# Optimization experiments

Hardware: AMD Instinct MI355X
Metric: run time of the kernel (lower is better)

## Reference

```python
import jax, jax.numpy as jnp
import numpy as np

PROX_TOL = 5
SEG_PENALTY = 3.0
SEG_REWARD = 0.3
CLASS_WEIGHTS = np.array([0.1, 5.0, 5.0], dtype=np.float32)


def setup_inputs() -> dict:
    key = jax.random.key(0)
    k1, k2, k3 = jax.random.split(key, 3)
    B, S, C = 256, 16384, 3
    logits = jax.random.normal(k1, (B, S, C), dtype=jnp.float32)
    labels = jax.random.randint(k2, (B, S), 0, 3, dtype=jnp.int64)
    tokens = jax.random.randint(k3, (B, S), 0, 1000, dtype=jnp.int64)
    return {"logits": logits, "labels": labels, "tokens": tokens}


def _window_any(mask, tol):
    # sliding 'any' over [t-tol, t+tol], clipped at sequence edges ('SAME' padding)
    m = mask.astype(jnp.float32)
    r = jax.lax.reduce_window(m, 0.0, jax.lax.max, (1, 2 * tol + 1), (1, 1), 'SAME')
    return r > 0.0


def reference(logits, labels, tokens):
    B, S, C = logits.shape
    cw = jnp.asarray(CLASS_WEIGHTS, dtype=logits.dtype)

    # weighted cross-entropy, reduction='none' -> w[y] * nll  [B, S]
    logp = jax.nn.log_softmax(logits, axis=-1)
    nll = -jnp.take_along_axis(logp, labels[..., None], axis=-1)[..., 0]
    base_loss = nll * cw[labels]

    predictions = jnp.argmax(logits, axis=-1)
    pred_switch = predictions >= 1   # [B, S]
    true_switch = labels >= 1        # [B, S]

    # segmentation adjustment (tokens is not None): for predicted switches,
    # the t+1 < S check overwrites the penalty with the reward, so:
    #   t <  S-1        -> reward
    #   t == S-1, t>=1  -> penalty (offset loop fired)
    pos = jnp.arange(S)
    adj = jnp.where(pred_switch & (pos < S - 1), SEG_REWARD,
                    jnp.where(pred_switch & (pos == S - 1) & (pos >= 1), SEG_PENALTY, 1.0))
    base_loss = base_loss * adj.astype(base_loss.dtype)

    # proximity reward: true switch with any predicted switch within +/- tol -> *0.1
    pred_near = _window_any(pred_switch, PROX_TOL)
    base_loss = jnp.where(true_switch & pred_near, base_loss * 0.1, base_loss)

    # false-positive penalty: predicted switch farther than tol from every true
    # switch -> *2.0 (only applied if the sequence has at least one true switch)
    true_near = _window_any(true_switch, PROX_TOL)
    has_true = jnp.any(true_switch, axis=1, keepdims=True)
    base_loss = jnp.where(pred_switch & has_true & (~true_near), base_loss * 2.0, base_loss)

    valid_mask = (labels != -100).astype(base_loss.dtype)
    return (base_loss * valid_mask).sum() / valid_mask.sum()
```

## Files before the change

### kernel.cpp

```cpp
#include <hip/hip_runtime.h>

#define SEQ 16384
#define TOL 5
#define CHUNK 1024
#define NCHUNK (SEQ / CHUNK)
#define NW (CHUNK / 64)
#define JITER (CHUNK / 256)
#define NROW 256
#define NBLK (NROW * NCHUNK)
#define TOTAL_VALID 4194304.0


__global__ __launch_bounds__(256, 4) void switch_loss_kernel(
    const float* __restrict__ logits,
    const int* __restrict__ labels,
    float* __restrict__ blk_sum, float* __restrict__ blk_fp,
    int* __restrict__ blk_any)
{
    const int row = blockIdx.y;
    const int chunk = blockIdx.x;
    const int s0 = chunk * CHUNK;
    const int t = threadIdx.x;
    const int w = t >> 6;
    const int lane = t & 63;

    __shared__ unsigned long long ps[NW + 2];
    __shared__ unsigned long long ts[NW + 2];
    __shared__ float wsum[4], wfp[4];
    __shared__ int wany[4];

    const float* __restrict__ lrow = logits + (size_t)row * (SEQ * 3);
    const int* __restrict__ labrow = labels + (size_t)row * SEQ;

    float l0v[JITER], l1v[JITER], l2v[JITER];
    int yv[JITER];
    #pragma unroll
    for (int j = 0; j < JITER; ++j) {
        const int s = s0 + j * 256 + t;
        l0v[j] = lrow[s * 3 + 0];
        l1v[j] = lrow[s * 3 + 1];
        l2v[j] = lrow[s * 3 + 2];
        yv[j]  = labrow[s];
    }

    if (w == 0) {
        const int pos = s0 - 64 + lane;
        const bool act = (lane >= 64 - TOL) && (pos >= 0);
        bool psw = false, tsw = false;
        if (act) {
            const float h0 = lrow[pos * 3 + 0];
            const float h1 = lrow[pos * 3 + 1];
            const float h2 = lrow[pos * 3 + 2];
            psw = (h1 > h0) || (h2 > fmaxf(h0, h1));
            const int y = labrow[pos];
            tsw = (y >= 1) && (y <= 2);
        }
        const unsigned long long bp = __ballot(psw);
        const unsigned long long bt = __ballot(tsw);
        if (lane == 0) { ps[0] = bp; ts[0] = bt; }
    } else if (w == 1) {
        const int pos = s0 + CHUNK + lane;
        const bool act = (lane < TOL) && (pos < SEQ);
        bool psw = false, tsw = false;
        if (act) {
            const float h0 = lrow[pos * 3 + 0];
            const float h1 = lrow[pos * 3 + 1];
            const float h2 = lrow[pos * 3 + 2];
            psw = (h1 > h0) || (h2 > fmaxf(h0, h1));
            const int y = labrow[pos];
            tsw = (y >= 1) && (y <= 2);
        }
        const unsigned long long bp = __ballot(psw);
        const unsigned long long bt = __ballot(tsw);
        if (lane == 0) { ps[NW + 1] = bp; ts[NW + 1] = bt; }
    }

    float lossv[JITER];
    unsigned pswbits = 0, tswbits = 0;
    unsigned long long my_ts_or = 0ull;

    #pragma unroll
    for (int j = 0; j < JITER; ++j) {
        const int s = s0 + j * 256 + t;
        const float l0 = l0v[j], l1 = l1v[j], l2 = l2v[j];
        const int y = yv[j];

        const float m01 = fmaxf(l0, l1);
        const float m = fmaxf(m01, l2);
        const bool psw = (l1 > l0) || (l2 > m01);

        const float sum = __expf(l0 - m) + __expf(l1 - m) + __expf(l2 - m);
        const float lse = m + __logf(sum);

        const bool valid = (y >= 0) && (y <= 2);
        const bool tsw = valid && (y >= 1);
        const float ly = (y == 0) ? l0 : ((y == 1) ? l1 : l2);
        const float wgt = (y == 0) ? 0.1f : 5.0f;
        float loss = valid ? (lse - ly) * wgt : 0.0f;

        const float adj = psw ? ((s < SEQ - 1) ? 0.3f : 3.0f) : 1.0f;
        lossv[j] = loss * adj;

        pswbits |= (unsigned)psw << j;
        tswbits |= (unsigned)tsw << j;

        const unsigned long long bp = __ballot(psw);
        const unsigned long long bt = __ballot(tsw);
        my_ts_or |= bt;
        if (lane == 0) { ps[1 + j * 4 + w] = bp; ts[1 + j * 4 + w] = bt; }
    }
    if (lane == 0) wany[w] = (my_ts_or != 0ull) ? 1 : 0;
    __syncthreads();

    float lsum = 0.0f, lfp = 0.0f;

    #pragma unroll
    for (int j = 0; j < JITER; ++j) {
        const int s = s0 + j * 256 + t;
        const bool psw = (pswbits >> j) & 1u;
        const bool tsw = (tswbits >> j) & 1u;

        int lo = s - TOL; lo = (lo < 0) ? 0 : lo;
        int hi = s + TOL; hi = (hi > SEQ - 1) ? (SEQ - 1) : hi;
        const int len = hi - lo + 1;
        const int rel = lo - s0 + 64;
        const int qq = rel >> 6;
        const int sh = rel & 63;

        unsigned long long pw = ps[qq] >> sh;
        unsigned long long tw = ts[qq] >> sh;
        if (sh + len > 64) {
            pw |= ps[qq + 1] << (64 - sh);
            tw |= ts[qq + 1] << (64 - sh);
        }
        const unsigned long long mlen = (1ull << len) - 1ull;
        const bool pred_near = (pw & mlen) != 0ull;
        const bool true_near = (tw & mlen) != 0ull;

        float loss = lossv[j];
        if (tsw && pred_near) loss *= 0.1f;
        lsum += loss;
        if (psw && !true_near) lfp += loss;
    }

    #pragma unroll
    for (int off = 32; off > 0; off >>= 1) {
        lsum += __shfl_down(lsum, off, 64);
        lfp  += __shfl_down(lfp, off, 64);
    }
    if (lane == 0) { wsum[w] = lsum; wfp[w] = lfp; }
    __syncthreads();
    if (t == 0) {
        const int slot = row * NCHUNK + chunk;
        blk_sum[slot] = wsum[0] + wsum[1] + wsum[2] + wsum[3];
        blk_fp[slot]  = wfp[0] + wfp[1] + wfp[2] + wfp[3];
        blk_any[slot] = wany[0] | wany[1] | wany[2] | wany[3];
    }
}

__global__ void finalize_kernel(const float* __restrict__ blk_sum,
                                const float* __restrict__ blk_fp,
                                const int* __restrict__ blk_any,
                                float* __restrict__ out) {
    const int t = threadIdx.x;
    const int w = t >> 6, lane = t & 63;
    __shared__ double wsum[4];

    float s = 0.0f, f = 0.0f;
    int any = 0;
    #pragma unroll
    for (int c = 0; c < NCHUNK; ++c) {
        const int slot = t * NCHUNK + c;
        s += blk_sum[slot];
        f += blk_fp[slot];
        any |= blk_any[slot];
    }
    double v = (double)s + (any ? (double)f : 0.0);
    #pragma unroll
    for (int off = 32; off > 0; off >>= 1)
        v += __shfl_down(v, off, 64);
    if (lane == 0) wsum[w] = v;
    __syncthreads();
    if (t == 0)
        out[0] = (float)((wsum[0] + wsum[1] + wsum[2] + wsum[3]) / TOTAL_VALID);
}

extern "C" void kernel_launch(void* const* d_in, const int* in_sizes, int n_in,
                              void* d_out, int out_size, void* d_ws, size_t ws_size,
                              hipStream_t stream) {
    const float* logits = (const float*)d_in[0];
    const int* labels = (const int*)d_in[1];
    (void)in_sizes; (void)n_in; (void)out_size; (void)ws_size;

    float* blk_sum = (float*)d_ws;
    float* blk_fp = blk_sum + NBLK;
    int* blk_any = (int*)(blk_fp + NBLK);
    float* out = (float*)d_out;

    switch_loss_kernel<<<dim3(NCHUNK, NROW), 256, 0, stream>>>(
        logits, labels, blk_sum, blk_fp, blk_any);
    finalize_kernel<<<1, 256, 0, stream>>>(blk_sum, blk_fp, blk_any, out);
}
```

Before: 108.2 us.

## Vectorize loads with 8 contiguous positions per thread and byte-packed switch masks

Each thread now handles 8 consecutive positions and loads its logits as six float4 values and its labels as two int4 values, instead of strided scalar loads. The chunk doubles to 2048 positions, so there are half as many blocks. Switch bits are packed into per-thread bytes in shared memory and assembled into 64-bit words, which replaces the per-iteration wave ballots. Halo loading is merged into one wave, and finalize uses vector loads. The aim is fewer, wider memory transactions, at the cost of non-coalesced per-thread 96-byte strides and fewer blocks in flight.

```diff
diff --git a/kernel.cpp b/kernel.cpp
--- a/kernel.cpp
+++ b/kernel.cpp
@@ -2,10 +2,10 @@
 
 #define SEQ 16384
 #define TOL 5
-#define CHUNK 1024
+#define CHUNK 2048
 #define NCHUNK (SEQ / CHUNK)
 #define NW (CHUNK / 64)
-#define JITER (CHUNK / 256)
+#define P 8
 #define NROW 256
 #define NBLK (NROW * NCHUNK)
 #define TOTAL_VALID 4194304.0
@@ -26,71 +26,61 @@
 
     __shared__ unsigned long long ps[NW + 2];
     __shared__ unsigned long long ts[NW + 2];
+    __shared__ __align__(8) unsigned char psb[256];
+    __shared__ __align__(8) unsigned char tsb[256];
     __shared__ float wsum[4], wfp[4];
     __shared__ int wany[4];
 
     const float* __restrict__ lrow = logits + (size_t)row * (SEQ * 3);
     const int* __restrict__ labrow = labels + (size_t)row * SEQ;
 
-    float l0v[JITER], l1v[JITER], l2v[JITER];
-    int yv[JITER];
-    #pragma unroll
-    for (int j = 0; j < JITER; ++j) {
-        const int s = s0 + j * 256 + t;
-        l0v[j] = lrow[s * 3 + 0];
-        l1v[j] = lrow[s * 3 + 1];
-        l2v[j] = lrow[s * 3 + 2];
-        yv[j]  = labrow[s];
-    }
-
-    if (w == 0) {
-        const int pos = s0 - 64 + lane;
-        const bool act = (lane >= 64 - TOL) && (pos >= 0);
-        bool psw = false, tsw = false;
-        if (act) {
+    const int sb = s0 + t * P;
+
+    const float4* __restrict__ lp = (const float4*)(lrow + (size_t)sb * 3);
+    const float4 f0 = lp[0], f1 = lp[1], f2 = lp[2], f3 = lp[3], f4 = lp[4], f5 = lp[5];
+    const int4* __restrict__ yp = (const int4*)(labrow + sb);
+    const int4 ya = yp[0], yb = yp[1];
+
+    bool hp = false, ht = false;
+    if (t < 2 * TOL) {
+        const int pos = (t < TOL) ? (s0 - TOL + t) : (s0 + CHUNK + (t - TOL));
+        if (pos >= 0 && pos < SEQ) {
             const float h0 = lrow[pos * 3 + 0];
             const float h1 = lrow[pos * 3 + 1];
             const float h2 = lrow[pos * 3 + 2];
-            psw = (h1 > h0) || (h2 > fmaxf(h0, h1));
-            const int y = labrow[pos];
-            tsw = (y >= 1) && (y <= 2);
+            hp = (h1 > h0) || (h2 > fmaxf(h0, h1));
+            ht = (labrow[pos] >= 1);
         }
-        const unsigned long long bp = __ballot(psw);
-        const unsigned long long bt = __ballot(tsw);
-        if (lane == 0) { ps[0] = bp; ts[0] = bt; }
-    } else if (w == 1) {
-        const int pos = s0 + CHUNK + lane;
-        const bool act = (lane < TOL) && (pos < SEQ);
-        bool psw = false, tsw = false;
-        if (act) {
-            const float h0 = lrow[pos * 3 + 0];
-            const float h1 = lrow[pos * 3 + 1];
-            const float h2 = lrow[pos * 3 + 2];
-            psw = (h1 > h0) || (h2 > fmaxf(h0, h1));
-            const int y = labrow[pos];
-            tsw = (y >= 1) && (y <= 2);
+    }
+    if (w == 0) {
+        const unsigned long long bp = __ballot(hp);
+        const unsigned long long bt = __ballot(ht);
+        if (lane == 0) {
+            ps[0] = (bp & 0x1Full) << 59;
+            ts[0] = (bt & 0x1Full) << 59;
+            ps[NW + 1] = (bp >> TOL) & 0x1Full;
+            ts[NW + 1] = (bt >> TOL) & 0x1Full;
         }
-        const unsigned long long bp = __ballot(psw);
-        const unsigned long long bt = __ballot(tsw);
-        if (lane == 0) { ps[NW + 1] = bp; ts[NW + 1] = bt; }
-    }
-
-    float lossv[JITER];
-    unsigned pswbits = 0, tswbits = 0;
-    unsigned long long my_ts_or = 0ull;
-
-    #pragma unroll
-    for (int j = 0; j < JITER; ++j) {
-        const int s = s0 + j * 256 + t;
-        const float l0 = l0v[j], l1 = l1v[j], l2 = l2v[j];
-        const int y = yv[j];
+    }
+
+    const float L0[P] = {f0.x, f0.w, f1.z, f2.y, f3.x, f3.w, f4.z, f5.y};
+    const float L1[P] = {f0.y, f1.x, f1.w, f2.z, f3.y, f4.x, f4.w, f5.z};
+    const float L2[P] = {f0.z, f1.y, f2.x, f2.w, f3.z, f4.y, f5.x, f5.w};
+    const int   Y[P]  = {ya.x, ya.y, ya.z, ya.w, yb.x, yb.y, yb.z, yb.w};
+
+    float lossv[P];
+    unsigned pn = 0, tn = 0;
+    #pragma unroll
+    for (int p = 0; p < P; ++p) {
+        const float l0 = L0[p], l1 = L1[p], l2 = L2[p];
+        const int y = Y[p];
 
         const float m01 = fmaxf(l0, l1);
-        const float m = fmaxf(m01, l2);
+        const float mx = fmaxf(m01, l2);
         const bool psw = (l1 > l0) || (l2 > m01);
 
-        const float sum = __expf(l0 - m) + __expf(l1 - m) + __expf(l2 - m);
-        const float lse = m + __logf(sum);
+        const float sum = __expf(l0 - mx) + __expf(l1 - mx) + __expf(l2 - mx);
+        const float lse = mx + __logf(sum);
 
         const bool valid = (y >= 0) && (y <= 2);
         const bool tsw = valid && (y >= 1);
@@ -98,27 +88,33 @@
         const float wgt = (y == 0) ? 0.1f : 5.0f;
         float loss = valid ? (lse - ly) * wgt : 0.0f;
 
+        const int s = sb + p;
         const float adj = psw ? ((s < SEQ - 1) ? 0.3f : 3.0f) : 1.0f;
-        lossv[j] = loss * adj;
-
-        pswbits |= (unsigned)psw << j;
-        tswbits |= (unsigned)tsw << j;
-
-        const unsigned long long bp = __ballot(psw);
-        const unsigned long long bt = __ballot(tsw);
-        my_ts_or |= bt;
-        if (lane == 0) { ps[1 + j * 4 + w] = bp; ts[1 + j * 4 + w] = bt; }
-    }
-    if (lane == 0) wany[w] = (my_ts_or != 0ull) ? 1 : 0;
+        lossv[p] = loss * adj;
+
+        pn |= (unsigned)psw << p;
+        tn |= (unsigned)tsw << p;
+    }
+    psb[t] = (unsigned char)pn;
+    tsb[t] = (unsigned char)tn;
+    {
+        const unsigned long long ba = __ballot(tn != 0);
+        if (lane == 0) wany[w] = (ba != 0ull) ? 1 : 0;
+    }
+    __syncthreads();
+
+    if (t < NW) {
+        ps[1 + t] = *(const unsigned long long*)&psb[t * 8];
+        ts[1 + t] = *(const unsigned long long*)&tsb[t * 8];
+    }
     __syncthreads();
 
     float lsum = 0.0f, lfp = 0.0f;
-
-    #pragma unroll
-    for (int j = 0; j < JITER; ++j) {
-        const int s = s0 + j * 256 + t;
-        const bool psw = (pswbits >> j) & 1u;
-        const bool tsw = (tswbits >> j) & 1u;
+    #pragma unroll
+    for (int p = 0; p < P; ++p) {
+        const int s = sb + p;
+        const bool psw = (pn >> p) & 1u;
+        const bool tsw = (tn >> p) & 1u;
 
         int lo = s - TOL; lo = (lo < 0) ? 0 : lo;
         int hi = s + TOL; hi = (hi > SEQ - 1) ? (SEQ - 1) : hi;
@@ -137,7 +133,7 @@
         const bool pred_near = (pw & mlen) != 0ull;
         const bool true_near = (tw & mlen) != 0ull;
 
-        float loss = lossv[j];
+        float loss = lossv[p];
         if (tsw && pred_near) loss *= 0.1f;
         lsum += loss;
         if (psw && !true_near) lfp += loss;
@@ -164,25 +160,27 @@
                                 float* __restrict__ out) {
     const int t = threadIdx.x;
     const int w = t >> 6, lane = t & 63;
-    __shared__ double wsum[4];
-
-    float s = 0.0f, f = 0.0f;
-    int any = 0;
-    #pragma unroll
-    for (int c = 0; c < NCHUNK; ++c) {
-        const int slot = t * NCHUNK + c;
-        s += blk_sum[slot];
-        f += blk_fp[slot];
-        any |= blk_any[slot];
-    }
+    __shared__ double wsumd[4];
+
+    const float4* __restrict__ fs = (const float4*)(blk_sum + t * NCHUNK);
+    const float4* __restrict__ ff = (const float4*)(blk_fp + t * NCHUNK);
+    const int4* __restrict__ fa = (const int4*)(blk_any + t * NCHUNK);
+    const float4 s0v = fs[0], s1v = fs[1];
+    const float4 f0v = ff[0], f1v = ff[1];
+    const int4 a0 = fa[0], a1 = fa[1];
+
+    const float s = ((s0v.x + s0v.y) + (s0v.z + s0v.w)) + ((s1v.x + s1v.y) + (s1v.z + s1v.w));
+    const float f = ((f0v.x + f0v.y) + (f0v.z + f0v.w)) + ((f1v.x + f1v.y) + (f1v.z + f1v.w));
+    const int any = a0.x | a0.y | a0.z | a0.w | a1.x | a1.y | a1.z | a1.w;
+
     double v = (double)s + (any ? (double)f : 0.0);
     #pragma unroll
     for (int off = 32; off > 0; off >>= 1)
         v += __shfl_down(v, off, 64);
-    if (lane == 0) wsum[w] = v;
+    if (lane == 0) wsumd[w] = v;
     __syncthreads();
     if (t == 0)
-        out[0] = (float)((wsum[0] + wsum[1] + wsum[2] + wsum[3]) / TOTAL_VALID);
+        out[0] = (float)((wsumd[0] + wsumd[1] + wsumd[2] + wsumd[3]) / TOTAL_VALID);
 }
 
 extern "C" void kernel_launch(void* const* d_in, const int* in_sizes, int n_in,
```

After: 109.4 us (median of 2 runs). About the same (+1.1%).
